# Kernel tuning notes

Measured on AMD Instinct MI355X. Metric: run time of the kernel, lower is better.

Reference implementation:

```python
import jax, jax.numpy as jnp
import numpy as np

B, T, H, V = 32, 256, 1024, 256


def setup_inputs() -> dict:
    key = jax.random.key(0)
    ks = jax.random.split(key, 12)
    xavier = float(np.sqrt(6.0 / (H + V)))
    inp = {
        "x": jax.random.randint(ks[0], (B, T), 0, V, dtype=jnp.int64),
        "targets": jax.random.randint(ks[1], (B, T), 0, V, dtype=jnp.int64),
        "h0": jnp.zeros((B, H), jnp.float32),
        "c0": jnp.zeros((B, H), jnp.float32),
        "h1": jnp.zeros((B, H), jnp.float32),
        "c1": jnp.zeros((B, H), jnp.float32),
        # learned params
        "emb": jax.random.normal(ks[2], (V, H), jnp.float32) * 0.05,
        "W_ih0": jax.random.normal(ks[3], (H, 4 * H), jnp.float32) / np.sqrt(H),
        "W_hh0": jax.random.normal(ks[4], (H, 4 * H), jnp.float32) / np.sqrt(H),
        "b0": jnp.zeros((4 * H,), jnp.float32),
        "W_ih1": jax.random.normal(ks[5], (H, 4 * H), jnp.float32) / np.sqrt(H),
        "W_hh1": jax.random.normal(ks[6], (H, 4 * H), jnp.float32) / np.sqrt(H),
        "b1": jnp.zeros((4 * H,), jnp.float32),
        "W_out": jax.random.uniform(ks[7], (H, V), jnp.float32, -xavier, xavier),
        "b_out": jnp.zeros((V,), jnp.float32),
    }
    return inp


def _lstm_cell(h, c, inp, W_ih, W_hh, b):
    # gates: [B, 4H] -> i, f, g, o
    z = inp @ W_ih + h @ W_hh + b
    i, f, g, o = jnp.split(z, 4, axis=-1)
    c_new = jax.nn.sigmoid(f) * c + jax.nn.sigmoid(i) * jnp.tanh(g)
    h_new = jax.nn.sigmoid(o) * jnp.tanh(c_new)
    return h_new, c_new


def reference(x, targets, h0, c0, h1, c1, emb, W_ih0, W_hh0, b0,
              W_ih1, W_hh1, b1, W_out, b_out):
    # Teacher-forcing branch: embed targets, feed embedding at every step.
    embeddings = emb[targets]            # [B, T, H]
    e_seq = jnp.swapaxes(embeddings, 0, 1)  # [T, B, H] for scan over time

    def step(carry, e_t):
        (h0, c0), (h1, c1) = carry
        h0, c0 = _lstm_cell(h0, c0, e_t, W_ih0, W_hh0, b0)
        h1, c1 = _lstm_cell(h1, c1, h0, W_ih1, W_hh1, b1)
        logit = h1 @ W_out + b_out       # [B, V]
        return ((h0, c0), (h1, c1)), logit

    carry0 = ((h0, c0), (h1, c1))
    carry_f, logits_tbv = jax.lax.scan(step, carry0, e_seq)
    logits = jnp.swapaxes(logits_tbv, 0, 1)  # [B, T, V]
    (h0f, c0f), (h1f, c1f) = carry_f
    return logits, h0f, c0f, h1f, c1f
```

## Files before the change

kernel.cpp:

```cpp
#include <hip/hip_runtime.h>
#include <cstdint>


typedef float    f32x4 __attribute__((ext_vector_type(4)));
typedef short    s16x8 __attribute__((ext_vector_type(8)));
typedef unsigned u32x4 __attribute__((ext_vector_type(4)));

#define DEV __device__ __forceinline__

DEV unsigned short f2bf(float x){
  unsigned u = __builtin_bit_cast(unsigned, x);
  unsigned r = (u + 0x7fffu + ((u >> 16) & 1u)) >> 16;
  return (unsigned short)r;
}
DEV float bf2f(unsigned short b){ return __builtin_bit_cast(float, ((unsigned)b) << 16); }

DEV s16x8 ld16(const void* p){ return *(const s16x8*)p; }

DEV f32x4 MF(s16x8 a, s16x8 b, f32x4 c){
  return __builtin_amdgcn_mfma_f32_16x16x32_bf16(a, b, c, 0, 0, 0);
}

#define LDC(dst, ptr)  asm volatile("global_load_dwordx4 %0, %1, off sc0 sc1" : "=v"(dst) : "v"(ptr))
#define LDP(dst, ptr)  asm volatile("global_load_dwordx4 %0, %1, off"         : "=v"(dst) : "v"(ptr))
#define WAITVM(n) do { asm volatile("s_waitcnt vmcnt(" #n ")" ::: "memory"); \
                       __builtin_amdgcn_sched_barrier(0); } while (0)
#define CFENCE()  asm volatile("" ::: "memory")
#define TRIPLE(Cmn, Ahm, Alm, Bhn, Bln) do { \
    Cmn = MF(Ahm, Bhn, Cmn); Cmn = MF(Ahm, Bln, Cmn); Cmn = MF(Alm, Bhn, Cmn); } while (0)

DEV void st16c(void* p, u32x4 v){
  asm volatile("global_store_dwordx4 %0, %1, off sc0 sc1" :: "v"(p), "v"(v) : "memory");
}
DEV void set_flag(int* p, int v){
  __hip_atomic_store(p, v, __ATOMIC_RELAXED, __HIP_MEMORY_SCOPE_AGENT);
}
template<int SLP>
DEV void pollT(const int* f, int lane, int target){
  const int* p0 = f + lane * 8;
  const int* p1 = f + (64 + lane) * 8;
  for (;;) {
    int a = __hip_atomic_load(p0, __ATOMIC_RELAXED, __HIP_MEMORY_SCOPE_AGENT);
    int b = __hip_atomic_load(p1, __ATOMIC_RELAXED, __HIP_MEMORY_SCOPE_AGENT);
    if (__all((a >= target) && (b >= target))) break;
    __builtin_amdgcn_s_sleep(SLP);
  }
  CFENCE();
}
DEV char* h0slot(char* wa0, char* s0, char* hi, int s){
  return (s == 0) ? s0 : ((s <= 128) ? wa0 + ((size_t)(s - 1) << 17)
                                     : hi  + ((size_t)(s - 129) << 17));
}

DEV void halfgemm8(const char* smemMat, const char* ALb, const char* Bb,
                   int wgl, int ksb, int lane, f32x4 (&C)[2][2]) {
  s16x8 P[3][4], AL[3][2];
  #pragma unroll
  for (int d = 0; d < 2; ++d) {
    #pragma unroll
    for (int q = 0; q < 4; ++q) LDP(P[d][q], Bb + ((q * 32 + ksb + d) << 10) + lane * 16);
    LDP(AL[d][0], ALb + ((((wgl * 2 + 0) * 2 + 1) * 32 + ksb + d) << 10) + lane * 16);
    LDP(AL[d][1], ALb + ((((wgl * 2 + 1) * 2 + 1) * 32 + ksb + d) << 10) + lane * 16);
  }
  #pragma unroll
  for (int i = 0; i < 8; ++i) {
    const int ks = ksb + i;
    if (i < 6) {
      #pragma unroll
      for (int q = 0; q < 4; ++q) LDP(P[(i + 2) % 3][q], Bb + ((q * 32 + ks + 2) << 10) + lane * 16);
      LDP(AL[(i + 2) % 3][0], ALb + ((((wgl * 2 + 0) * 2 + 1) * 32 + ks + 2) << 10) + lane * 16);
      LDP(AL[(i + 2) % 3][1], ALb + ((((wgl * 2 + 1) * 2 + 1) * 32 + ks + 2) << 10) + lane * 16);
    }
    s16x8 Ah0 = ld16(smemMat + ((0 * 32 + ks) << 10) + lane * 16);
    s16x8 Ah1 = ld16(smemMat + ((1 * 32 + ks) << 10) + lane * 16);
    if (i < 6) { WAITVM(12); } else if (i == 6) { WAITVM(6); } else { WAITVM(0); }
    TRIPLE(C[0][0], Ah0, AL[i % 3][0], P[i % 3][0], P[i % 3][2]);
    TRIPLE(C[0][1], Ah0, AL[i % 3][0], P[i % 3][1], P[i % 3][3]);
    TRIPLE(C[1][0], Ah1, AL[i % 3][1], P[i % 3][0], P[i % 3][2]);
    TRIPLE(C[1][1], Ah1, AL[i % 3][1], P[i % 3][1], P[i % 3][3]);
  }
}

__global__ void prep_wfrag(const float* __restrict__ W0, const float* __restrict__ W1,
                           const float* __restrict__ W2, const float* __restrict__ W3,
                           char* D0, char* D1, char* D2, char* D3) {
  int gid = blockIdx.x * 256 + threadIdx.x;
  int lane = gid & 63, ks = (gid >> 6) & 31, jb = (gid >> 11) & 255, mat = gid >> 19;
  const float* S = (mat == 0) ? W0 : (mat == 1) ? W1 : (mat == 2) ? W2 : W3;
  char* D = (mat == 0) ? D0 : (mat == 1) ? D1 : (mat == 2) ? D2 : D3;
  int jp = jb * 16 + (lane & 15), u = jp >> 2, g = jp & 3;
  int kb = ks * 32 + (lane >> 4) * 8;
  s16x8 vh, vl;
  #pragma unroll
  for (int i = 0; i < 8; ++i) {
    float x = S[(kb + i) * 4096 + g * 1024 + u];
    unsigned short h = f2bf(x);
    vh[i] = (short)h;
    vl[i] = (short)f2bf(x - bf2f(h));
  }
  *(s16x8*)(D + (((jb * 2 + 0) * 32 + ks) << 10) + lane * 16) = vh;
  *(s16x8*)(D + (((jb * 2 + 1) * 32 + ks) << 10) + lane * 16) = vl;
}

__global__ void prep_bfrag(const float* __restrict__ emb, const float* __restrict__ Wout,
                           char* Demb, char* Dwout) {
  int gid = blockIdx.x * 256 + threadIdx.x;
  int lane = gid & 63, ks = (gid >> 6) & 31, vb = (gid >> 11) & 15, which = gid >> 15;
  int v = vb * 16 + (lane & 15), kb = ks * 32 + (lane >> 4) * 8;
  s16x8 vh, vl;
  #pragma unroll
  for (int i = 0; i < 8; ++i) {
    float x = which ? Wout[(kb + i) * 256 + v] : emb[v * 1024 + kb + i];
    unsigned short h = f2bf(x);
    vh[i] = (short)h;
    vl[i] = (short)f2bf(x - bf2f(h));
  }
  char* D = which ? Dwout : Demb;
  *(s16x8*)(D + (((vb * 2 + 0) * 32 + ks) << 10) + lane * 16) = vh;
  *(s16x8*)(D + (((vb * 2 + 1) * 32 + ks) << 10) + lane * 16) = vl;
}

__global__ void prep_hinit(const float* __restrict__ h0, const float* __restrict__ h1,
                           char* h0s0, char* h1f) {
  int gid = blockIdx.x * 256 + threadIdx.x;
  int lane = gid & 63, ks = (gid >> 6) & 31, nt = (gid >> 11) & 1, which = gid >> 12;
  const float* S = which ? h1 : h0;
  char* D = which ? h1f : h0s0;
  int b = nt * 16 + (lane & 15), kb = ks * 32 + (lane >> 4) * 8;
  s16x8 vh, vl;
  #pragma unroll
  for (int i = 0; i < 8; ++i) {
    float x = S[b * 1024 + kb + i];
    unsigned short h = f2bf(x);
    vh[i] = (short)h;
    vl[i] = (short)f2bf(x - bf2f(h));
  }
  *(s16x8*)(D + (((0 * 2 + nt) * 32 + ks) << 10) + lane * 16) = vh;
  *(s16x8*)(D + (((1 * 2 + nt) * 32 + ks) << 10) + lane * 16) = vl;
}

__global__ void prep_misc(const float* __restrict__ b1, float* b1i, int* f0a, int* f1a) {
  int i = blockIdx.x * 256 + threadIdx.x;
  if (i < 4096) b1i[i] = b1[(i & 3) * 1024 + (i >> 2)];
  if (i < 1024) { f0a[i] = -1; f1a[i] = -1; }
}

__global__ __launch_bounds__(256, 1) void lstm_persist(
    const int* __restrict__ tgt,
    const float* __restrict__ c0_in, const float* __restrict__ c1_in,
    const float* __restrict__ b0, const float* __restrict__ b_out,
    char* __restrict__ WA0, const char* __restrict__ WA1, const char* __restrict__ WA2,
    const char* __restrict__ WAi0, const char* __restrict__ WoutB, const char* __restrict__ embB,
    float* __restrict__ E0, const float* __restrict__ b1i,
    char* __restrict__ h0s0, char* __restrict__ h0hi, char* __restrict__ h1frag,
    int* __restrict__ f0, int* __restrict__ f1,
    float* __restrict__ out)
{
  extern __shared__ char smem[];
  constexpr int PART = 131072;
  constexpr int RP   = 131072 + 16384;
  const int tid = threadIdx.x, lane = tid & 63, wv = tid >> 6;
  const int wg = blockIdx.x;
  const bool isL0 = (wg < 128);
  const int wgl = isL0 ? wg : (wg - 128);
  const int l15 = lane & 15, l4 = lane >> 4;
  const int mi_e = wv >> 1, nt_e = wv & 1;

  __builtin_amdgcn_fence(__ATOMIC_ACQUIRE, "agent");

  if (isL0) {
    u32x4 tmp[8];
    for (int blk = 0; blk < 4; ++blk) {
      #pragma unroll
      for (int q = 0; q < 8; ++q) {
        int idx = tid + (blk * 8 + q) * 256;
        int l16 = idx & 63, ks = (idx >> 6) & 31, mi = (idx >> 11) & 1, part = idx >> 12;
        LDC(tmp[q], WA0 + ((((wgl * 2 + mi) * 2 + part) * 32 + ks) << 10) + l16 * 16);
      }
      WAITVM(0);
      #pragma unroll
      for (int q = 0; q < 8; ++q) {
        int idx = tid + (blk * 8 + q) * 256;
        int l16 = idx & 63, ks = (idx >> 6) & 31, mi = (idx >> 11) & 1, part = idx >> 12;
        *(u32x4*)(smem + (((part * 2 + mi) * 32 + ks) << 10) + l16 * 16) = tmp[q];
      }
    }
  } else {
    for (int idx = tid; idx < 8192; idx += 256) {
      int l16 = idx & 63, ks = (idx >> 6) & 31, mi = (idx >> 11) & 1, mat = idx >> 12;
      const char* W = mat ? WA2 : WA1;
      u32x4 v = *(const u32x4*)(W + ((((wgl * 2 + mi) * 2 + 0) * 32 + ks) << 10) + l16 * 16);
      *(u32x4*)(smem + (((mat * 2 + mi) * 32 + ks) << 10) + l16 * 16) = v;
    }
  }

  if (isL0) {
    f32x4 C[2][4];
    #pragma unroll
    for (int a = 0; a < 2; ++a)
      #pragma unroll
      for (int b = 0; b < 4; ++b) C[a][b] = 0.0f;
    for (int ks = 0; ks < 32; ++ks) {
      s16x8 Ah0, Ah1, Al0, Al1;
      LDC(Ah0, WAi0 + ((((wgl * 2 + 0) * 2 + 0) * 32 + ks) << 10) + lane * 16);
      LDC(Ah1, WAi0 + ((((wgl * 2 + 1) * 2 + 0) * 32 + ks) << 10) + lane * 16);
      LDC(Al0, WAi0 + ((((wgl * 2 + 0) * 2 + 1) * 32 + ks) << 10) + lane * 16);
      LDC(Al1, WAi0 + ((((wgl * 2 + 1) * 2 + 1) * 32 + ks) << 10) + lane * 16);
      WAITVM(0);
      #pragma unroll
      for (int v4 = 0; v4 < 4; ++v4) {
        int vb = wv * 4 + v4;
        s16x8 Bh = ld16(embB + (((vb * 2 + 0) * 32 + ks) << 10) + lane * 16);
        s16x8 Bl = ld16(embB + (((vb * 2 + 1) * 32 + ks) << 10) + lane * 16);
        TRIPLE(C[0][v4], Ah0, Al0, Bh, Bl);
        TRIPLE(C[1][v4], Ah1, Al1, Bh, Bl);
      }
    }
    #pragma unroll
    for (int mi = 0; mi < 2; ++mi) {
      int jb4 = wgl * 32 + mi * 16 + l4 * 4;
      int u = jb4 >> 2;
      f32x4 bb;
      #pragma unroll
      for (int r = 0; r < 4; ++r) bb[r] = b0[r * 1024 + u];
      #pragma unroll
      for (int v4 = 0; v4 < 4; ++v4) {
        int v = (wv * 4 + v4) * 16 + l15;
        *(f32x4*)(E0 + v * 4096 + jb4) = C[mi][v4] + bb;
      }
    }
  }

  float cst;
  {
    const float* cs = isL0 ? c0_in : c1_in;
    cst = cs[(nt_e * 16 + l15) * 1024 + wgl * 8 + mi_e * 4 + l4];
  }
  f32x4 b1z = {0.f, 0.f, 0.f, 0.f};
  if (!isL0) b1z = *(const f32x4*)(b1i + wgl * 32 + mi_e * 16 + (l4 << 2));

  __syncthreads();
  if (tid == 0) set_flag((isL0 ? f0 : f1) + wgl * 8, 0);

  if (isL0) {
    for (int t = 0; t < 256; ++t) {
      const int s = t + 1;
      f32x4 C[2][2];
      #pragma unroll
      for (int a = 0; a < 2; ++a)
        #pragma unroll
        for (int b = 0; b < 2; ++b) C[a][b] = 0.0f;

      int tv = tgt[(nt_e * 16 + l15) * 256 + t];
      f32x4 e0v = *(const f32x4*)(E0 + (size_t)tv * 4096 + wgl * 32 + mi_e * 16 + (l4 << 2));
      pollT<1>(f0, lane, t);
      const char* Bb = h0slot(WA0, h0s0, h0hi, t);
      const int ksb = wv * 8;
      s16x8 P[3][4];
      #pragma unroll
      for (int d = 0; d < 2; ++d)
        #pragma unroll
        for (int q = 0; q < 4; ++q) LDP(P[d][q], Bb + ((q * 32 + ksb + d) << 10) + lane * 16);
      #pragma unroll
      for (int i = 0; i < 8; ++i) {
        const int ks = ksb + i;
        if (i < 6) {
          #pragma unroll
          for (int q = 0; q < 4; ++q) LDP(P[(i + 2) % 3][q], Bb + ((q * 32 + ks + 2) << 10) + lane * 16);
        }
        s16x8 Ah0 = ld16(smem + ((0 * 32 + ks) << 10) + lane * 16);
        s16x8 Ah1 = ld16(smem + ((1 * 32 + ks) << 10) + lane * 16);
        s16x8 Al0 = ld16(smem + ((2 * 32 + ks) << 10) + lane * 16);
        s16x8 Al1 = ld16(smem + ((3 * 32 + ks) << 10) + lane * 16);
        if (i < 6) { WAITVM(8); } else if (i == 6) { WAITVM(4); } else { WAITVM(0); }
        TRIPLE(C[0][0], Ah0, Al0, P[i % 3][0], P[i % 3][2]);
        TRIPLE(C[0][1], Ah0, Al0, P[i % 3][1], P[i % 3][3]);
        TRIPLE(C[1][0], Ah1, Al1, P[i % 3][0], P[i % 3][2]);
        TRIPLE(C[1][1], Ah1, Al1, P[i % 3][1], P[i % 3][3]);
      }

      #pragma unroll
      for (int mi = 0; mi < 2; ++mi)
        #pragma unroll
        for (int nt = 0; nt < 2; ++nt)
          *(f32x4*)(smem + PART + ((wv * 4 + mi * 2 + nt) << 10) + lane * 16) = C[mi][nt];
      __syncthreads();

      {
        f32x4 z = *(const f32x4*)(smem + PART + ((0 * 4 + wv) << 10) + lane * 16);
        #pragma unroll
        for (int w = 1; w < 4; ++w)
          z += *(const f32x4*)(smem + PART + ((w * 4 + wv) << 10) + lane * 16);
        z += e0v;
        float ig = 1.f / (1.f + __expf(-z[0]));
        float fg = 1.f / (1.f + __expf(-z[1]));
        float og = 1.f / (1.f + __expf(-z[3]));
        float cn = fg * cst + ig * tanhf(z[2]);
        float hn = og * tanhf(cn);
        cst = cn;
        unsigned short hb = f2bf(hn);
        unsigned short lb = f2bf(hn - bf2f(hb));
        *(short*)(smem + RP + ((0 + nt_e) * 16 + l15) * 16 + (mi_e * 4 + l4) * 2) = (short)hb;
        *(short*)(smem + RP + ((2 + nt_e) * 16 + l15) * 16 + (mi_e * 4 + l4) * 2) = (short)lb;
        if (t == 255) {
          int u = wgl * 8 + mi_e * 4 + l4, b = nt_e * 16 + l15;
          out[2097152 + b * 1024 + u] = hn;
          out[2097152 + 32768 + b * 1024 + u] = cn;
        }
      }
      __syncthreads();

      if (wv == 0) {
        char* hd = h0slot(WA0, h0s0, h0hi, s);
        u32x4 v = *(const u32x4*)(smem + RP + lane * 16);
        char* dst = hd + (((lane >> 4) * 32 + (wgl >> 2)) << 10) + ((wgl & 3) * 16 + l15) * 16;
        st16c(dst, v);
        asm volatile("s_waitcnt vmcnt(0)" ::: "memory");
        if (lane == 0) set_flag(f0 + wgl * 8, s);
      }
    }
  } else {
    f32x4 zpre;
    {
      pollT<2>(f0, lane, 1);
      f32x4 C2[2][2];
      #pragma unroll
      for (int a = 0; a < 2; ++a)
        #pragma unroll
        for (int b = 0; b < 2; ++b) C2[a][b] = 0.0f;
      halfgemm8(smem, WA1, h0slot(WA0, h0s0, h0hi, 1), wgl, wv * 8, lane, C2);
      #pragma unroll
      for (int mi = 0; mi < 2; ++mi)
        #pragma unroll
        for (int nt = 0; nt < 2; ++nt)
          *(f32x4*)(smem + PART + ((wv * 4 + mi * 2 + nt) << 10) + lane * 16) = C2[mi][nt];
      __syncthreads();
      zpre = *(const f32x4*)(smem + PART + ((0 * 4 + wv) << 10) + lane * 16);
      #pragma unroll
      for (int w = 1; w < 4; ++w)
        zpre += *(const f32x4*)(smem + PART + ((w * 4 + wv) << 10) + lane * 16);
      __syncthreads();
    }

    for (int t = 0; t < 256; ++t) {
      const int s = t + 1;
      f32x4 C[2][2];
      #pragma unroll
      for (int a = 0; a < 2; ++a)
        #pragma unroll
        for (int b = 0; b < 2; ++b) C[a][b] = 0.0f;

      pollT<1>(f1, lane, t);
      halfgemm8(smem + 65536, WA2, h1frag + (size_t)t * 131072, wgl, wv * 8, lane, C);

      #pragma unroll
      for (int mi = 0; mi < 2; ++mi)
        #pragma unroll
        for (int nt = 0; nt < 2; ++nt)
          *(f32x4*)(smem + PART + ((wv * 4 + mi * 2 + nt) << 10) + lane * 16) = C[mi][nt];
      __syncthreads();

      {
        f32x4 z = *(const f32x4*)(smem + PART + ((0 * 4 + wv) << 10) + lane * 16);
        #pragma unroll
        for (int w = 1; w < 4; ++w)
          z += *(const f32x4*)(smem + PART + ((w * 4 + wv) << 10) + lane * 16);
        z += zpre + b1z;
        float ig = 1.f / (1.f + __expf(-z[0]));
        float fg = 1.f / (1.f + __expf(-z[1]));
        float og = 1.f / (1.f + __expf(-z[3]));
        float cn = fg * cst + ig * tanhf(z[2]);
        float hn = og * tanhf(cn);
        cst = cn;
        unsigned short hb = f2bf(hn);
        unsigned short lb = f2bf(hn - bf2f(hb));
        *(short*)(smem + RP + ((0 + nt_e) * 16 + l15) * 16 + (mi_e * 4 + l4) * 2) = (short)hb;
        *(short*)(smem + RP + ((2 + nt_e) * 16 + l15) * 16 + (mi_e * 4 + l4) * 2) = (short)lb;
        if (t == 255) {
          int u = wgl * 8 + mi_e * 4 + l4, b = nt_e * 16 + l15;
          out[2097152 + 65536 + b * 1024 + u] = hn;
          out[2097152 + 65536 + 32768 + b * 1024 + u] = cn;
        }
      }
      __syncthreads();

      if (wv == 0) {
        char* hd = h1frag + (size_t)s * 131072;
        u32x4 v = *(const u32x4*)(smem + RP + lane * 16);
        char* dst = hd + (((lane >> 4) * 32 + (wgl >> 2)) << 10) + ((wgl & 3) * 16 + l15) * 16;
        st16c(dst, v);
        asm volatile("s_waitcnt vmcnt(0)" ::: "memory");
        if (lane == 0) set_flag(f1 + wgl * 8, s);
      }

      if (t < 255) {
        pollT<2>(f0, lane, t + 2);
        f32x4 C2[2][2];
        #pragma unroll
        for (int a = 0; a < 2; ++a)
          #pragma unroll
          for (int b = 0; b < 2; ++b) C2[a][b] = 0.0f;
        halfgemm8(smem, WA1, h0slot(WA0, h0s0, h0hi, t + 2), wgl, wv * 8, lane, C2);
        #pragma unroll
        for (int mi = 0; mi < 2; ++mi)
          #pragma unroll
          for (int nt = 0; nt < 2; ++nt)
            *(f32x4*)(smem + PART + ((wv * 4 + mi * 2 + nt) << 10) + lane * 16) = C2[mi][nt];
        __syncthreads();
        zpre = *(const f32x4*)(smem + PART + ((0 * 4 + wv) << 10) + lane * 16);
        #pragma unroll
        for (int w = 1; w < 4; ++w)
          zpre += *(const f32x4*)(smem + PART + ((w * 4 + wv) << 10) + lane * 16);
        __syncthreads();
      }
    }
  }

  {
    const int tp = isL0 ? wgl : (128 + wgl);
    pollT<32>(f1, lane, tp + 1);
    const char* A = h1frag + (size_t)(tp + 1) * 131072;
    f32x4 C[2][4];
    #pragma unroll
    for (int a = 0; a < 2; ++a)
      #pragma unroll
      for (int b = 0; b < 4; ++b) C[a][b] = 0.0f;
    s16x8 QA[4], QB[4];
    #pragma unroll
    for (int q = 0; q < 4; ++q) LDP(QA[q], A + ((q * 32 + 0) << 10) + lane * 16);
    for (int kk = 0; kk < 16; ++kk) {
      const int ks = kk * 2;
      #pragma unroll
      for (int q = 0; q < 4; ++q) LDP(QB[q], A + ((q * 32 + ks + 1) << 10) + lane * 16);
      asm volatile("s_waitcnt vmcnt(4)" ::: "memory");
      __builtin_amdgcn_sched_barrier(0);
      #pragma unroll
      for (int v4 = 0; v4 < 4; ++v4) {
        int vb = wv * 4 + v4;
        s16x8 Bh = ld16(WoutB + (((vb * 2 + 0) * 32 + ks) << 10) + lane * 16);
        s16x8 Bl = ld16(WoutB + (((vb * 2 + 1) * 32 + ks) << 10) + lane * 16);
        C[0][v4] = MF(QA[0], Bh, C[0][v4]); C[0][v4] = MF(QA[0], Bl, C[0][v4]); C[0][v4] = MF(QA[2], Bh, C[0][v4]);
        C[1][v4] = MF(QA[1], Bh, C[1][v4]); C[1][v4] = MF(QA[1], Bl, C[1][v4]); C[1][v4] = MF(QA[3], Bh, C[1][v4]);
      }
      if (kk < 15) {
        #pragma unroll
        for (int q = 0; q < 4; ++q) LDP(QA[q], A + ((q * 32 + ks + 2) << 10) + lane * 16);
        asm volatile("s_waitcnt vmcnt(4)" ::: "memory");
      } else {
        asm volatile("s_waitcnt vmcnt(0)" ::: "memory");
      }
      __builtin_amdgcn_sched_barrier(0);
      #pragma unroll
      for (int v4 = 0; v4 < 4; ++v4) {
        int vb = wv * 4 + v4;
        s16x8 Bh = ld16(WoutB + (((vb * 2 + 0) * 32 + ks + 1) << 10) + lane * 16);
        s16x8 Bl = ld16(WoutB + (((vb * 2 + 1) * 32 + ks + 1) << 10) + lane * 16);
        C[0][v4] = MF(QB[0], Bh, C[0][v4]); C[0][v4] = MF(QB[0], Bl, C[0][v4]); C[0][v4] = MF(QB[2], Bh, C[0][v4]);
        C[1][v4] = MF(QB[1], Bh, C[1][v4]); C[1][v4] = MF(QB[1], Bl, C[1][v4]); C[1][v4] = MF(QB[3], Bh, C[1][v4]);
      }
    }
    #pragma unroll
    for (int nt = 0; nt < 2; ++nt)
      #pragma unroll
      for (int v4 = 0; v4 < 4; ++v4) {
        int v = (wv * 4 + v4) * 16 + l15;
        float bo = b_out[v];
        #pragma unroll
        for (int r = 0; r < 4; ++r) {
          int b = nt * 16 + l4 * 4 + r;
          out[((size_t)b * 256 + tp) * 256 + v] = C[nt][v4][r] + bo;
        }
      }
  }
}

extern "C" void kernel_launch(void* const* d_in, const int* in_sizes, int n_in,
                              void* d_out, int out_size, void* d_ws, size_t ws_size,
                              hipStream_t stream) {
  const int*   targets = (const int*)d_in[1];
  const float* h0_in   = (const float*)d_in[2];
  const float* c0_in   = (const float*)d_in[3];
  const float* h1_in   = (const float*)d_in[4];
  const float* c1_in   = (const float*)d_in[5];
  const float* emb     = (const float*)d_in[6];
  const float* W_ih0   = (const float*)d_in[7];
  const float* W_hh0   = (const float*)d_in[8];
  const float* b0      = (const float*)d_in[9];
  const float* W_ih1   = (const float*)d_in[10];
  const float* W_hh1   = (const float*)d_in[11];
  const float* b1      = (const float*)d_in[12];
  const float* W_out   = (const float*)d_in[13];
  const float* b_out   = (const float*)d_in[14];
  float* out = (float*)d_out;

  char* ws = (char*)d_ws;
  char*  WA0    = ws;
  char*  WA1    = ws + 16777216;
  char*  WA2    = ws + 33554432;
  char*  WoutB  = ws + 50331648;
  char*  embB   = ws + 51380224;
  float* E0     = (float*)(ws + 52428800);
  float* b1i    = (float*)(ws + 56623104);
  int*   f0     = (int*)(ws + 56639488);
  int*   f1     = (int*)(ws + 56643584);
  char*  h0s0   = ws + 56647680;
  char*  h0hi   = ws + 56778752;
  char*  h1frag = ws + 73555968;
  char*  WAi0   = h1frag + 16777216;

  prep_misc <<<18,   256, 0, stream>>>(b1, b1i, f0, f1);
  prep_wfrag<<<8192, 256, 0, stream>>>(W_hh0, W_ih1, W_hh1, W_ih0, WA0, WA1, WA2, WAi0);
  prep_bfrag<<<256,  256, 0, stream>>>(emb, W_out, embB, WoutB);
  prep_hinit<<<32,   256, 0, stream>>>(h0_in, h1_in, h0s0, h1frag);

  hipFuncSetAttribute(reinterpret_cast<const void*>(lstm_persist),
                      hipFuncAttributeMaxDynamicSharedMemorySize, 148480);
  lstm_persist<<<256, 256, 148480, stream>>>(
      targets, c0_in, c1_in, b0, b_out,
      WA0, WA1, WA2, WAi0, WoutB, embB,
      E0, b1i, h0s0, h0hi, h1frag, f0, f1, out);
}
```

Before: 1.729 ms.

## Double block to 512 threads and split layer-1 input/recurrent GEMMs across wave groups

```diff
diff --git a/kernel.cpp b/kernel.cpp
--- a/kernel.cpp
+++ b/kernel.cpp
@@ -78,6 +78,37 @@
     TRIPLE(C[0][1], Ah0, AL[i % 3][0], P[i % 3][1], P[i % 3][3]);
     TRIPLE(C[1][0], Ah1, AL[i % 3][1], P[i % 3][0], P[i % 3][2]);
     TRIPLE(C[1][1], Ah1, AL[i % 3][1], P[i % 3][1], P[i % 3][3]);
+  }
+}
+
+DEV void gemm8g(const char* Ab, const char* Bb,
+                int wgl, int ksb, int lane, f32x4 (&C)[2][2]) {
+  s16x8 P[3][4], AH[3][2], AL[3][2];
+  #pragma unroll
+  for (int d = 0; d < 2; ++d) {
+    #pragma unroll
+    for (int q = 0; q < 4; ++q) LDP(P[d][q], Bb + ((q * 32 + ksb + d) << 10) + lane * 16);
+    LDP(AH[d][0], Ab + ((((wgl * 2 + 0) * 2 + 0) * 32 + ksb + d) << 10) + lane * 16);
+    LDP(AH[d][1], Ab + ((((wgl * 2 + 1) * 2 + 0) * 32 + ksb + d) << 10) + lane * 16);
+    LDP(AL[d][0], Ab + ((((wgl * 2 + 0) * 2 + 1) * 32 + ksb + d) << 10) + lane * 16);
+    LDP(AL[d][1], Ab + ((((wgl * 2 + 1) * 2 + 1) * 32 + ksb + d) << 10) + lane * 16);
+  }
+  #pragma unroll
+  for (int i = 0; i < 8; ++i) {
+    const int ks = ksb + i;
+    if (i < 6) {
+      #pragma unroll
+      for (int q = 0; q < 4; ++q) LDP(P[(i + 2) % 3][q], Bb + ((q * 32 + ks + 2) << 10) + lane * 16);
+      LDP(AH[(i + 2) % 3][0], Ab + ((((wgl * 2 + 0) * 2 + 0) * 32 + ks + 2) << 10) + lane * 16);
+      LDP(AH[(i + 2) % 3][1], Ab + ((((wgl * 2 + 1) * 2 + 0) * 32 + ks + 2) << 10) + lane * 16);
+      LDP(AL[(i + 2) % 3][0], Ab + ((((wgl * 2 + 0) * 2 + 1) * 32 + ks + 2) << 10) + lane * 16);
+      LDP(AL[(i + 2) % 3][1], Ab + ((((wgl * 2 + 1) * 2 + 1) * 32 + ks + 2) << 10) + lane * 16);
+    }
+    if (i < 6) { WAITVM(16); } else if (i == 6) { WAITVM(8); } else { WAITVM(0); }
+    TRIPLE(C[0][0], AH[i % 3][0], AL[i % 3][0], P[i % 3][0], P[i % 3][2]);
+    TRIPLE(C[0][1], AH[i % 3][0], AL[i % 3][0], P[i % 3][1], P[i % 3][3]);
+    TRIPLE(C[1][0], AH[i % 3][1], AL[i % 3][1], P[i % 3][0], P[i % 3][2]);
+    TRIPLE(C[1][1], AH[i % 3][1], AL[i % 3][1], P[i % 3][1], P[i % 3][3]);
   }
 }
 
@@ -145,7 +176,7 @@
   if (i < 1024) { f0a[i] = -1; f1a[i] = -1; }
 }
 
-__global__ __launch_bounds__(256, 1) void lstm_persist(
+__global__ __launch_bounds__(512, 1) void lstm_persist(
     const int* __restrict__ tgt,
     const float* __restrict__ c0_in, const float* __restrict__ c1_in,
     const float* __restrict__ b0, const float* __restrict__ b_out,
@@ -157,49 +188,50 @@
     float* __restrict__ out)
 {
   extern __shared__ char smem[];
-  constexpr int PART = 131072;
-  constexpr int RP   = 131072 + 16384;
+  constexpr int PARTA = 131072;
+  constexpr int ZTMP  = 65536;
+  constexpr int ZC    = 81920;
+  constexpr int RP    = 147456;
   const int tid = threadIdx.x, lane = tid & 63, wv = tid >> 6;
   const int wg = blockIdx.x;
   const bool isL0 = (wg < 128);
   const int wgl = isL0 ? wg : (wg - 128);
   const int l15 = lane & 15, l4 = lane >> 4;
-  const int mi_e = wv >> 1, nt_e = wv & 1;
+  const int mi_e = (wv >> 1) & 1, nt_e = wv & 1;
 
   __builtin_amdgcn_fence(__ATOMIC_ACQUIRE, "agent");
 
   if (isL0) {
     u32x4 tmp[8];
-    for (int blk = 0; blk < 4; ++blk) {
+    for (int blk = 0; blk < 2; ++blk) {
       #pragma unroll
       for (int q = 0; q < 8; ++q) {
-        int idx = tid + (blk * 8 + q) * 256;
+        int idx = tid + (blk * 8 + q) * 512;
         int l16 = idx & 63, ks = (idx >> 6) & 31, mi = (idx >> 11) & 1, part = idx >> 12;
         LDC(tmp[q], WA0 + ((((wgl * 2 + mi) * 2 + part) * 32 + ks) << 10) + l16 * 16);
       }
       WAITVM(0);
       #pragma unroll
       for (int q = 0; q < 8; ++q) {
-        int idx = tid + (blk * 8 + q) * 256;
+        int idx = tid + (blk * 8 + q) * 512;
         int l16 = idx & 63, ks = (idx >> 6) & 31, mi = (idx >> 11) & 1, part = idx >> 12;
         *(u32x4*)(smem + (((part * 2 + mi) * 32 + ks) << 10) + l16 * 16) = tmp[q];
       }
     }
   } else {
-    for (int idx = tid; idx < 8192; idx += 256) {
-      int l16 = idx & 63, ks = (idx >> 6) & 31, mi = (idx >> 11) & 1, mat = idx >> 12;
-      const char* W = mat ? WA2 : WA1;
-      u32x4 v = *(const u32x4*)(W + ((((wgl * 2 + mi) * 2 + 0) * 32 + ks) << 10) + l16 * 16);
-      *(u32x4*)(smem + (((mat * 2 + mi) * 32 + ks) << 10) + l16 * 16) = v;
+    for (int idx = tid; idx < 4096; idx += 512) {
+      int l16 = idx & 63, ks = (idx >> 6) & 31, mi = idx >> 11;
+      u32x4 v = *(const u32x4*)(WA2 + ((((wgl * 2 + mi) * 2 + 0) * 32 + ks) << 10) + l16 * 16);
+      *(u32x4*)(smem + ((mi * 32 + ks) << 10) + l16 * 16) = v;
     }
   }
 
   if (isL0) {
-    f32x4 C[2][4];
+    f32x4 C[2][2];
     #pragma unroll
     for (int a = 0; a < 2; ++a)
       #pragma unroll
-      for (int b = 0; b < 4; ++b) C[a][b] = 0.0f;
+      for (int b = 0; b < 2; ++b) C[a][b] = 0.0f;
     for (int ks = 0; ks < 32; ++ks) {
       s16x8 Ah0, Ah1, Al0, Al1;
       LDC(Ah0, WAi0 + ((((wgl * 2 + 0) * 2 + 0) * 32 + ks) << 10) + lane * 16);
@@ -208,8 +240,8 @@
       LDC(Al1, WAi0 + ((((wgl * 2 + 1) * 2 + 1) * 32 + ks) << 10) + lane * 16);
       WAITVM(0);
       #pragma unroll
-      for (int v4 = 0; v4 < 4; ++v4) {
-        int vb = wv * 4 + v4;
+      for (int v4 = 0; v4 < 2; ++v4) {
+        int vb = wv * 2 + v4;
         s16x8 Bh = ld16(embB + (((vb * 2 + 0) * 32 + ks) << 10) + lane * 16);
         s16x8 Bl = ld16(embB + (((vb * 2 + 1) * 32 + ks) << 10) + lane * 16);
         TRIPLE(C[0][v4], Ah0, Al0, Bh, Bl);
@@ -224,20 +256,20 @@
       #pragma unroll
       for (int r = 0; r < 4; ++r) bb[r] = b0[r * 1024 + u];
       #pragma unroll
-      for (int v4 = 0; v4 < 4; ++v4) {
-        int v = (wv * 4 + v4) * 16 + l15;
+      for (int v4 = 0; v4 < 2; ++v4) {
+        int v = (wv * 2 + v4) * 16 + l15;
         *(f32x4*)(E0 + v * 4096 + jb4) = C[mi][v4] + bb;
       }
     }
   }
 
-  float cst;
-  {
+  float cst = 0.f;
+  f32x4 b1z = {0.f, 0.f, 0.f, 0.f};
+  if (wv < 4) {
     const float* cs = isL0 ? c0_in : c1_in;
     cst = cs[(nt_e * 16 + l15) * 1024 + wgl * 8 + mi_e * 4 + l4];
-  }
-  f32x4 b1z = {0.f, 0.f, 0.f, 0.f};
-  if (!isL0) b1z = *(const f32x4*)(b1i + wgl * 32 + mi_e * 16 + (l4 << 2));
+    if (!isL0) b1z = *(const f32x4*)(b1i + wgl * 32 + mi_e * 16 + (l4 << 2));
+  }
 
   __syncthreads();
   if (tid == 0) set_flag((isL0 ? f0 : f1) + wgl * 8, 0);
@@ -251,20 +283,23 @@
         #pragma unroll
         for (int b = 0; b < 2; ++b) C[a][b] = 0.0f;
 
-      int tv = tgt[(nt_e * 16 + l15) * 256 + t];
-      f32x4 e0v = *(const f32x4*)(E0 + (size_t)tv * 4096 + wgl * 32 + mi_e * 16 + (l4 << 2));
+      f32x4 e0v = {0.f, 0.f, 0.f, 0.f};
+      if (wv < 4) {
+        int tv = tgt[(nt_e * 16 + l15) * 256 + t];
+        e0v = *(const f32x4*)(E0 + (size_t)tv * 4096 + wgl * 32 + mi_e * 16 + (l4 << 2));
+      }
       pollT<1>(f0, lane, t);
       const char* Bb = h0slot(WA0, h0s0, h0hi, t);
-      const int ksb = wv * 8;
+      const int ksb = wv * 4;
       s16x8 P[3][4];
       #pragma unroll
       for (int d = 0; d < 2; ++d)
         #pragma unroll
         for (int q = 0; q < 4; ++q) LDP(P[d][q], Bb + ((q * 32 + ksb + d) << 10) + lane * 16);
       #pragma unroll
-      for (int i = 0; i < 8; ++i) {
+      for (int i = 0; i < 4; ++i) {
         const int ks = ksb + i;
-        if (i < 6) {
+        if (i < 2) {
           #pragma unroll
           for (int q = 0; q < 4; ++q) LDP(P[(i + 2) % 3][q], Bb + ((q * 32 + ks + 2) << 10) + lane * 16);
         }
@@ -272,25 +307,36 @@
         s16x8 Ah1 = ld16(smem + ((1 * 32 + ks) << 10) + lane * 16);
         s16x8 Al0 = ld16(smem + ((2 * 32 + ks) << 10) + lane * 16);
         s16x8 Al1 = ld16(smem + ((3 * 32 + ks) << 10) + lane * 16);
-        if (i < 6) { WAITVM(8); } else if (i == 6) { WAITVM(4); } else { WAITVM(0); }
+        if (i < 2) { WAITVM(8); } else if (i == 2) { WAITVM(4); } else { WAITVM(0); }
         TRIPLE(C[0][0], Ah0, Al0, P[i % 3][0], P[i % 3][2]);
         TRIPLE(C[0][1], Ah0, Al0, P[i % 3][1], P[i % 3][3]);
         TRIPLE(C[1][0], Ah1, Al1, P[i % 3][0], P[i % 3][2]);
         TRIPLE(C[1][1], Ah1, Al1, P[i % 3][1], P[i % 3][3]);
       }
 
-      #pragma unroll
-      for (int mi = 0; mi < 2; ++mi)
-        #pragma unroll
-        for (int nt = 0; nt < 2; ++nt)
-          *(f32x4*)(smem + PART + ((wv * 4 + mi * 2 + nt) << 10) + lane * 16) = C[mi][nt];
+      if (wv >= 4) {
+        #pragma unroll
+        for (int mi = 0; mi < 2; ++mi)
+          #pragma unroll
+          for (int nt = 0; nt < 2; ++nt)
+            *(f32x4*)(smem + PARTA + (((wv - 4) * 4 + mi * 2 + nt) << 10) + lane * 16) = C[mi][nt];
+      }
       __syncthreads();
-
-      {
-        f32x4 z = *(const f32x4*)(smem + PART + ((0 * 4 + wv) << 10) + lane * 16);
-        #pragma unroll
-        for (int w = 1; w < 4; ++w)
-          z += *(const f32x4*)(smem + PART + ((w * 4 + wv) << 10) + lane * 16);
+      if (wv < 4) {
+        #pragma unroll
+        for (int mi = 0; mi < 2; ++mi)
+          #pragma unroll
+          for (int nt = 0; nt < 2; ++nt) {
+            f32x4* p = (f32x4*)(smem + PARTA + ((wv * 4 + mi * 2 + nt) << 10) + lane * 16);
+            *p = *p + C[mi][nt];
+          }
+      }
+      __syncthreads();
+      if (wv < 4) {
+        f32x4 z = {0.f, 0.f, 0.f, 0.f};
+        #pragma unroll
+        for (int w = 0; w < 4; ++w)
+          z += *(const f32x4*)(smem + PARTA + ((w * 4 + wv) << 10) + lane * 16);
         z += e0v;
         float ig = 1.f / (1.f + __expf(-z[0]));
         float fg = 1.f / (1.f + __expf(-z[1]));
@@ -320,52 +366,66 @@
       }
     }
   } else {
-    f32x4 zpre;
-    {
+    if (wv >= 4) {
       pollT<2>(f0, lane, 1);
       f32x4 C2[2][2];
       #pragma unroll
       for (int a = 0; a < 2; ++a)
         #pragma unroll
         for (int b = 0; b < 2; ++b) C2[a][b] = 0.0f;
-      halfgemm8(smem, WA1, h0slot(WA0, h0s0, h0hi, 1), wgl, wv * 8, lane, C2);
+      gemm8g(WA1, h0slot(WA0, h0s0, h0hi, 1), wgl, (wv - 4) * 8, lane, C2);
       #pragma unroll
       for (int mi = 0; mi < 2; ++mi)
         #pragma unroll
         for (int nt = 0; nt < 2; ++nt)
-          *(f32x4*)(smem + PART + ((wv * 4 + mi * 2 + nt) << 10) + lane * 16) = C2[mi][nt];
-      __syncthreads();
-      zpre = *(const f32x4*)(smem + PART + ((0 * 4 + wv) << 10) + lane * 16);
-      #pragma unroll
-      for (int w = 1; w < 4; ++w)
-        zpre += *(const f32x4*)(smem + PART + ((w * 4 + wv) << 10) + lane * 16);
-      __syncthreads();
-    }
+          *(f32x4*)(smem + ZTMP + (((wv - 4) * 4 + mi * 2 + nt) << 10) + lane * 16) = C2[mi][nt];
+    }
+    __syncthreads();
+    if (wv >= 4) {
+      const int q = wv - 4;
+      f32x4 zq = {0.f, 0.f, 0.f, 0.f};
+      #pragma unroll
+      for (int w = 0; w < 4; ++w)
+        zq += *(const f32x4*)(smem + ZTMP + ((w * 4 + q) << 10) + lane * 16);
+      *(f32x4*)(smem + ZC + ((0 * 4 + q) << 10) + lane * 16) = zq;
+    }
+    __syncthreads();
 
     for (int t = 0; t < 256; ++t) {
       const int s = t + 1;
+      const int cur = t & 1, nxt = cur ^ 1;
       f32x4 C[2][2];
       #pragma unroll
       for (int a = 0; a < 2; ++a)
         #pragma unroll
         for (int b = 0; b < 2; ++b) C[a][b] = 0.0f;
 
-      pollT<1>(f1, lane, t);
-      halfgemm8(smem + 65536, WA2, h1frag + (size_t)t * 131072, wgl, wv * 8, lane, C);
-
-      #pragma unroll
-      for (int mi = 0; mi < 2; ++mi)
-        #pragma unroll
-        for (int nt = 0; nt < 2; ++nt)
-          *(f32x4*)(smem + PART + ((wv * 4 + mi * 2 + nt) << 10) + lane * 16) = C[mi][nt];
+      if (wv < 4) {
+        pollT<1>(f1, lane, t);
+        halfgemm8(smem, WA2, h1frag + (size_t)t * 131072, wgl, wv * 8, lane, C);
+        #pragma unroll
+        for (int mi = 0; mi < 2; ++mi)
+          #pragma unroll
+          for (int nt = 0; nt < 2; ++nt)
+            *(f32x4*)(smem + PARTA + ((wv * 4 + mi * 2 + nt) << 10) + lane * 16) = C[mi][nt];
+      } else if (t < 255) {
+        pollT<2>(f0, lane, t + 2);
+        gemm8g(WA1, h0slot(WA0, h0s0, h0hi, t + 2), wgl, (wv - 4) * 8, lane, C);
+        #pragma unroll
+        for (int mi = 0; mi < 2; ++mi)
+          #pragma unroll
+          for (int nt = 0; nt < 2; ++nt)
+            *(f32x4*)(smem + ZTMP + (((wv - 4) * 4 + mi * 2 + nt) << 10) + lane * 16) = C[mi][nt];
+      }
       __syncthreads();
 
-      {
-        f32x4 z = *(const f32x4*)(smem + PART + ((0 * 4 + wv) << 10) + lane * 16);
-        #pragma unroll
-        for (int w = 1; w < 4; ++w)
-          z += *(const f32x4*)(smem + PART + ((w * 4 + wv) << 10) + lane * 16);
-        z += zpre + b1z;
+      if (wv < 4) {
+        f32x4 z = {0.f, 0.f, 0.f, 0.f};
+        #pragma unroll
+        for (int w = 0; w < 4; ++w)
+          z += *(const f32x4*)(smem + PARTA + ((w * 4 + wv) << 10) + lane * 16);
+        z += *(const f32x4*)(smem + ZC + ((cur * 4 + wv) << 10) + lane * 16);
+        z += b1z;
         float ig = 1.f / (1.f + __expf(-z[0]));
         float fg = 1.f / (1.f + __expf(-z[1]));
         float og = 1.f / (1.f + __expf(-z[3]));
@@ -381,6 +441,13 @@
           out[2097152 + 65536 + b * 1024 + u] = hn;
           out[2097152 + 65536 + 32768 + b * 1024 + u] = cn;
         }
+      } else if (t < 255) {
+        const int q = wv - 4;
+        f32x4 zq = {0.f, 0.f, 0.f, 0.f};
+        #pragma unroll
+        for (int w = 0; w < 4; ++w)
+          zq += *(const f32x4*)(smem + ZTMP + ((w * 4 + q) << 10) + lane * 16);
+        *(f32x4*)(smem + ZC + ((nxt * 4 + q) << 10) + lane * 16) = zq;
       }
       __syncthreads();
 
@@ -392,27 +459,6 @@
         asm volatile("s_waitcnt vmcnt(0)" ::: "memory");
         if (lane == 0) set_flag(f1 + wgl * 8, s);
       }
-
-      if (t < 255) {
-        pollT<2>(f0, lane, t + 2);
-        f32x4 C2[2][2];
-        #pragma unroll
-        for (int a = 0; a < 2; ++a)
-          #pragma unroll
-          for (int b = 0; b < 2; ++b) C2[a][b] = 0.0f;
-        halfgemm8(smem, WA1, h0slot(WA0, h0s0, h0hi, t + 2), wgl, wv * 8, lane, C2);
-        #pragma unroll
-        for (int mi = 0; mi < 2; ++mi)
-          #pragma unroll
-          for (int nt = 0; nt < 2; ++nt)
-            *(f32x4*)(smem + PART + ((wv * 4 + mi * 2 + nt) << 10) + lane * 16) = C2[mi][nt];
-        __syncthreads();
-        zpre = *(const f32x4*)(smem + PART + ((0 * 4 + wv) << 10) + lane * 16);
-        #pragma unroll
-        for (int w = 1; w < 4; ++w)
-          zpre += *(const f32x4*)(smem + PART + ((w * 4 + wv) << 10) + lane * 16);
-        __syncthreads();
-      }
     }
   }
 
@@ -420,11 +466,11 @@
     const int tp = isL0 ? wgl : (128 + wgl);
     pollT<32>(f1, lane, tp + 1);
     const char* A = h1frag + (size_t)(tp + 1) * 131072;
-    f32x4 C[2][4];
+    f32x4 C[2][2];
     #pragma unroll
     for (int a = 0; a < 2; ++a)
       #pragma unroll
-      for (int b = 0; b < 4; ++b) C[a][b] = 0.0f;
+      for (int b = 0; b < 2; ++b) C[a][b] = 0.0f;
     s16x8 QA[4], QB[4];
     #pragma unroll
     for (int q = 0; q < 4; ++q) LDP(QA[q], A + ((q * 32 + 0) << 10) + lane * 16);
@@ -435,8 +481,8 @@
       asm volatile("s_waitcnt vmcnt(4)" ::: "memory");
       __builtin_amdgcn_sched_barrier(0);
       #pragma unroll
-      for (int v4 = 0; v4 < 4; ++v4) {
-        int vb = wv * 4 + v4;
+      for (int v4 = 0; v4 < 2; ++v4) {
+        int vb = wv * 2 + v4;
         s16x8 Bh = ld16(WoutB + (((vb * 2 + 0) * 32 + ks) << 10) + lane * 16);
         s16x8 Bl = ld16(WoutB + (((vb * 2 + 1) * 32 + ks) << 10) + lane * 16);
         C[0][v4] = MF(QA[0], Bh, C[0][v4]); C[0][v4] = MF(QA[0], Bl, C[0][v4]); C[0][v4] = MF(QA[2], Bh, C[0][v4]);
@@ -451,8 +497,8 @@
       }
       __builtin_amdgcn_sched_barrier(0);
       #pragma unroll
-      for (int v4 = 0; v4 < 4; ++v4) {
-        int vb = wv * 4 + v4;
+      for (int v4 = 0; v4 < 2; ++v4) {
+        int vb = wv * 2 + v4;
         s16x8 Bh = ld16(WoutB + (((vb * 2 + 0) * 32 + ks + 1) << 10) + lane * 16);
         s16x8 Bl = ld16(WoutB + (((vb * 2 + 1) * 32 + ks + 1) << 10) + lane * 16);
         C[0][v4] = MF(QB[0], Bh, C[0][v4]); C[0][v4] = MF(QB[0], Bl, C[0][v4]); C[0][v4] = MF(QB[2], Bh, C[0][v4]);
@@ -462,8 +508,8 @@
     #pragma unroll
     for (int nt = 0; nt < 2; ++nt)
       #pragma unroll
-      for (int v4 = 0; v4 < 4; ++v4) {
-        int v = (wv * 4 + v4) * 16 + l15;
+      for (int v4 = 0; v4 < 2; ++v4) {
+        int v = (wv * 2 + v4) * 16 + l15;
         float bo = b_out[v];
         #pragma unroll
         for (int r = 0; r < 4; ++r) {
@@ -515,7 +561,7 @@
 
   hipFuncSetAttribute(reinterpret_cast<const void*>(lstm_persist),
                       hipFuncAttributeMaxDynamicSharedMemorySize, 148480);
-  lstm_persist<<<256, 256, 148480, stream>>>(
+  lstm_persist<<<256, 512, 148480, stream>>>(
       targets, c0_in, c1_in, b0, b_out,
       WA0, WA1, WA2, WAi0, WoutB, embB,
       E0, b1i, h0s0, h0hi, h1frag, f0, f1, out);
```

After: 3.393 ms. 1.96x slower.
